# Performance work log

Hardware: AMD Instinct MI355X
Metric: run time of the kernel (lower is better)

## Reference

```python
import jax, jax.numpy as jnp
import numpy as np

NU, NI, NB, D = 100000, 50000, 20000, 64
E_UI, E_UB, E_BI = 1_000_000, 600_000, 400_000
BATCH = 2048
NUM_LAYERS = 2
C_TEMP = 0.25


def _sym_laplacian(src, dst, n_src_offset, n_total):
    # bipartite graph made symmetric: edges (u, off+v) and (off+v, u), val 1.0
    row = np.concatenate([src, n_src_offset + dst])
    col = np.concatenate([n_src_offset + dst, src])
    deg = np.bincount(row, minlength=n_total).astype(np.float64)
    val = 1.0 / ((np.sqrt(deg[row]) + 1e-8) * (np.sqrt(deg[col]) + 1e-8))
    return row.astype(np.int32), col.astype(np.int32), val.astype(np.float32)


def setup_inputs() -> dict:
    rng = np.random.default_rng(0)
    ui_u = rng.integers(0, NU, E_UI)
    ui_i = rng.integers(0, NI, E_UI)
    ub_u = rng.integers(0, NU, E_UB)
    ub_b = rng.integers(0, NB, E_UB)
    bi_b = rng.integers(0, NB, E_BI)
    bi_i = rng.integers(0, NI, E_BI)

    il_row, il_col, il_val = _sym_laplacian(ui_u, ui_i, NU, NU + NI)
    bl_row, bl_col, bl_val = _sym_laplacian(ub_u, ub_b, NU, NU + NB)
    deg_b = np.bincount(bi_b, minlength=NB).astype(np.float64)
    agg_val = (1.0 / (deg_b + 1e-8))[bi_b].astype(np.float32)

    key = jax.random.key(0)
    k1, k2, k3 = jax.random.split(key, 3)
    std = 0.05  # xavier-ish init scale
    return {
        "users_feature": jax.random.normal(k1, (NU, D), jnp.float32) * std,
        "items_feature": jax.random.normal(k2, (NI, D), jnp.float32) * std,
        "bundles_feature": jax.random.normal(k3, (NB, D), jnp.float32) * std,
        "il_row": jnp.asarray(il_row), "il_col": jnp.asarray(il_col), "il_val": jnp.asarray(il_val),
        "bl_row": jnp.asarray(bl_row), "bl_col": jnp.asarray(bl_col), "bl_val": jnp.asarray(bl_val),
        "agg_row": jnp.asarray(bi_b.astype(np.int32)), "agg_col": jnp.asarray(bi_i.astype(np.int32)),
        "agg_val": jnp.asarray(agg_val),
        "users": jnp.asarray(rng.integers(0, NU, BATCH).astype(np.int32)),
        "bundles": jnp.asarray(rng.integers(0, NB, (BATCH, 2)).astype(np.int32)),
    }


def _spmm(row, col, val, feat, n):
    # COO SpMM: out[r] += val * feat[c]   (gather + segment-sum, memory bound)
    return jax.ops.segment_sum(val[:, None] * feat[col], row, num_segments=n)


def _one_propagate(row, col, val, A, B):
    f = jnp.concatenate([A, B], axis=0)
    n = f.shape[0]
    acc = f
    for i in range(NUM_LAYERS):
        f = _spmm(row, col, val, f, n) / (i + 2)
        nrm = jnp.maximum(jnp.linalg.norm(f, axis=1, keepdims=True), 1e-12)
        acc = acc + f / nrm
    return acc[: A.shape[0]], acc[A.shape[0]:]


def _c_loss(pos, aug):
    pos = pos / jnp.maximum(jnp.linalg.norm(pos, axis=1, keepdims=True), 1e-12)
    aug = aug / jnp.maximum(jnp.linalg.norm(aug, axis=1, keepdims=True), 1e-12)
    pos_score = jnp.sum(pos * aug, axis=1) / C_TEMP
    ttl = (pos @ aug.T) / C_TEMP
    return -jnp.mean(pos_score - jax.scipy.special.logsumexp(ttl, axis=1))


def reference(users_feature, items_feature, bundles_feature,
              il_row, il_col, il_val, bl_row, bl_col, bl_val,
              agg_row, agg_col, agg_val, users, bundles):
    # item-level propagation over symmetric (U+I) graph
    IL_u, IL_i = _one_propagate(il_row, il_col, il_val, users_feature, items_feature)
    # bundle rep from item-level: row-normalized [B,I] spmm
    IL_b = _spmm(agg_row, agg_col, agg_val, IL_i, bundles_feature.shape[0])
    # bundle-level propagation over symmetric (U+B) graph
    BL_u, BL_b = _one_propagate(bl_row, bl_col, bl_val, users_feature, bundles_feature)

    # BPR on (pos, neg) bundle pairs, summing both views
    pred = (jnp.sum(IL_u[users][:, None, :] * IL_b[bundles], axis=-1)
            + jnp.sum(BL_u[users][:, None, :] * BL_b[bundles], axis=-1))  # [BATCH, 2]
    bpr_loss = jnp.mean(jax.nn.softplus(pred[:, 1] - pred[:, 0]))  # -log sigmoid(pos-neg)

    c_loss = 0.5 * (_c_loss(IL_u[users], BL_u[users]) + _c_loss(IL_b[bundles[:, 0]], BL_b[bundles[:, 0]]))
    return jnp.stack([bpr_loss, c_loss])
```

## Files before the change

### kernel.cpp

```cpp
#include <hip/hip_runtime.h>
#include <hip/hip_fp16.h>
#include <math.h>

#define DD 64
#define INV_TEMP 4.0f
#define MAXBINS 1280
#define BINSHIFT 8
#define CAP 10240
#define ECAP2 (CAP / 512)
#define ECAP_A 16
#define COLBITS 18
#define COLMASK ((1u << COLBITS) - 1)
#define CBSHIFT 14
#define K1 32.0f
#define K2_OVER_K1 4.0f

typedef float v2f __attribute__((ext_vector_type(2)));

__device__ __forceinline__ float waveSum(float x) {
#pragma unroll
    for (int off = 32; off > 0; off >>= 1) x += __shfl_xor(x, off, 64);
    return x;
}

__device__ __forceinline__ unsigned packH2(float a, float b) {
    __half2 h = __halves2half2(__float2half_rn(a), __float2half_rn(b));
    return *(unsigned*)&h;
}
__device__ __forceinline__ float2 unpackH2(unsigned u) {
    __half2 h = *(__half2*)&u;
    return __half22float2(h);
}
__device__ __forceinline__ unsigned packFp8x4(float a, float b, float c, float d) {
    int v = __builtin_amdgcn_cvt_pk_fp8_f32(a, b, 0, false);
    v = __builtin_amdgcn_cvt_pk_fp8_f32(c, d, v, true);
    return (unsigned)v;
}

__device__ __forceinline__ void accFp8(uint4 d,
    v2f& a0, v2f& a1, v2f& a2, v2f& a3,
    v2f& a4, v2f& a5, v2f& a6, v2f& a7)
{
    a0 += __builtin_amdgcn_cvt_pk_f32_fp8((int)d.x, false);
    a1 += __builtin_amdgcn_cvt_pk_f32_fp8((int)d.x, true);
    a2 += __builtin_amdgcn_cvt_pk_f32_fp8((int)d.y, false);
    a3 += __builtin_amdgcn_cvt_pk_f32_fp8((int)d.y, true);
    a4 += __builtin_amdgcn_cvt_pk_f32_fp8((int)d.z, false);
    a5 += __builtin_amdgcn_cvt_pk_f32_fp8((int)d.z, true);
    a6 += __builtin_amdgcn_cvt_pk_f32_fp8((int)d.w, false);
    a7 += __builtin_amdgcn_cvt_pk_f32_fp8((int)d.w, true);
}

__device__ __forceinline__ void accH16(uint4 d,
    v2f& a0, v2f& a1, v2f& a2, v2f& a3)
{
    float2 h0 = unpackH2(d.x), h1 = unpackH2(d.y);
    float2 h2 = unpackH2(d.z), h3 = unpackH2(d.w);
    a0[0] += h0.x; a0[1] += h0.y; a1[0] += h1.x; a1[1] += h1.y;
    a2[0] += h2.x; a2[1] += h2.y; a3[0] += h3.x; a3[1] += h3.y;
}

__device__ __forceinline__ void zero4(uint4& d) { d.x = 0; d.y = 0; d.z = 0; d.w = 0; }

__device__ __forceinline__ void gatherFp8(
    const int* __restrict__ csp, int deg,
    const unsigned* __restrict__ tab, int sub,
    v2f& a0, v2f& a1, v2f& a2, v2f& a3,
    v2f& a4, v2f& a5, v2f& a6, v2f& a7)
{
    if (deg <= 0) return;
    int c0 = csp[0];
    int c1 = (1 < deg) ? csp[1] : 0;
    int c2 = (2 < deg) ? csp[2] : 0;
    int c3 = (3 < deg) ? csp[3] : 0;
    int c4 = (4 < deg) ? csp[4] : 0;
    int c5 = (5 < deg) ? csp[5] : 0;
    int c6 = (6 < deg) ? csp[6] : 0;
    int c7 = (7 < deg) ? csp[7] : 0;
    int kc = 0, k = 8;
    while (true) {
        uint4 d0 = *((const uint4*)(tab + (size_t)c0 * 16) + sub);
        uint4 d1 = *((const uint4*)(tab + (size_t)c1 * 16) + sub);
        uint4 d2 = *((const uint4*)(tab + (size_t)c2 * 16) + sub);
        uint4 d3 = *((const uint4*)(tab + (size_t)c3 * 16) + sub);
        uint4 d4 = *((const uint4*)(tab + (size_t)c4 * 16) + sub);
        uint4 d5 = *((const uint4*)(tab + (size_t)c5 * 16) + sub);
        uint4 d6 = *((const uint4*)(tab + (size_t)c6 * 16) + sub);
        uint4 d7 = *((const uint4*)(tab + (size_t)c7 * 16) + sub);
        bool more = k < deg;
        int n0 = 0, n1 = 0, n2 = 0, n3 = 0, n4 = 0, n5 = 0, n6 = 0, n7 = 0;
        if (more) {
            n0 = csp[k];
            n1 = (k + 1 < deg) ? csp[k + 1] : 0;
            n2 = (k + 2 < deg) ? csp[k + 2] : 0;
            n3 = (k + 3 < deg) ? csp[k + 3] : 0;
            n4 = (k + 4 < deg) ? csp[k + 4] : 0;
            n5 = (k + 5 < deg) ? csp[k + 5] : 0;
            n6 = (k + 6 < deg) ? csp[k + 6] : 0;
            n7 = (k + 7 < deg) ? csp[k + 7] : 0;
        }
        if (kc + 1 >= deg) zero4(d1);
        if (kc + 2 >= deg) zero4(d2);
        if (kc + 3 >= deg) zero4(d3);
        if (kc + 4 >= deg) zero4(d4);
        if (kc + 5 >= deg) zero4(d5);
        if (kc + 6 >= deg) zero4(d6);
        if (kc + 7 >= deg) zero4(d7);
        accFp8(d0, a0, a1, a2, a3, a4, a5, a6, a7);
        accFp8(d1, a0, a1, a2, a3, a4, a5, a6, a7);
        accFp8(d2, a0, a1, a2, a3, a4, a5, a6, a7);
        accFp8(d3, a0, a1, a2, a3, a4, a5, a6, a7);
        accFp8(d4, a0, a1, a2, a3, a4, a5, a6, a7);
        accFp8(d5, a0, a1, a2, a3, a4, a5, a6, a7);
        accFp8(d6, a0, a1, a2, a3, a4, a5, a6, a7);
        accFp8(d7, a0, a1, a2, a3, a4, a5, a6, a7);
        if (!more) break;
        c0 = n0; c1 = n1; c2 = n2; c3 = n3;
        c4 = n4; c5 = n5; c6 = n6; c7 = n7;
        kc = k; k += 8;
    }
}


__device__ __forceinline__ void fetchEdge(
    int i, const int* __restrict__ r1, const int* __restrict__ c1,
    const int* __restrict__ r2, const int* __restrict__ c2,
    const int* __restrict__ r3, const int* __restrict__ c3,
    int E1, int E12, int b2, int b3, int& row, int& col)
{
    if (i < E1)       { row = __builtin_nontemporal_load(&r1[i]);
                        col = __builtin_nontemporal_load(&c1[i]); }
    else if (i < E12) { int j = i - E1;
                        row = b2 + __builtin_nontemporal_load(&r2[j]);
                        col = __builtin_nontemporal_load(&c2[j]); }
    else              { int j = i - E12;
                        row = b3 + __builtin_nontemporal_load(&r3[j]);
                        col = __builtin_nontemporal_load(&c3[j]); }
}

__global__ void __launch_bounds__(1024)
binA_kernel(
    const int* __restrict__ r1, const int* __restrict__ c1,
    const int* __restrict__ r2, const int* __restrict__ c2,
    const int* __restrict__ r3, const int* __restrict__ c3,
    int E1, int E2, int E3, int b2, int b3, int nbins,
    int* __restrict__ binCursor, unsigned* __restrict__ binned,
    int chunk, int Etot)
{
    __shared__ int hist[MAXBINS];
    __shared__ int resv[MAXBINS];
    int t = threadIdx.x;
    for (int b = t; b < nbins; b += 1024) hist[b] = 0;
    __syncthreads();
    int lo = blockIdx.x * chunk;
    int hi = min(lo + chunk, Etot);
    int E12 = E1 + E2;
    int rowR[ECAP_A], colR[ECAP_A];
#pragma unroll
    for (int j = 0; j < ECAP_A; j++) {
        int i = lo + t + (j << 10);
        if (i < hi) {
            int row, col;
            fetchEdge(i, r1, c1, r2, c2, r3, c3, E1, E12, b2, b3, row, col);
            rowR[j] = row; colR[j] = col;
            atomicAdd(&hist[row >> BINSHIFT], 1);
        }
    }
    __syncthreads();
    for (int b = t; b < nbins; b += 1024) {
        int h = hist[b];
        resv[b] = h ? atomicAdd(&binCursor[b], h) : 0;
    }
    __syncthreads();
    for (int b = t; b < nbins; b += 1024) hist[b] = 0;
    __syncthreads();
#pragma unroll
    for (int j = 0; j < ECAP_A; j++) {
        int i = lo + t + (j << 10);
        if (i < hi) {
            int row = rowR[j], col = colR[j];
            int b = row >> BINSHIFT;
            int off = atomicAdd(&hist[b], 1);
            unsigned v = ((unsigned)(row & 255) << COLBITS) | (unsigned)col;
            binned[(size_t)b * CAP + resv[b] + off] = v;
        }
    }
}

__global__ void __launch_bounds__(512) binB_kernel(
    unsigned* __restrict__ binned, const int* __restrict__ binCursor,
    int ntot,
    int* __restrict__ cnt, int* __restrict__ rowStart)
{
    __shared__ int hist[4096];
    __shared__ int tsum[512];
    __shared__ int wtot[8];
    int b = blockIdx.x;
    size_t base = (size_t)b * CAP;
    int len = min(binCursor[b], CAP);
    int rowLo = b << BINSHIFT;
    int t = threadIdx.x;
#pragma unroll
    for (int i = 0; i < 8; i++) hist[t * 8 + i] = 0;
    __syncthreads();

    unsigned ent[ECAP2];
#pragma unroll
    for (int k = 0; k < ECAP2; k++) {
        int i = t + (k << 9);
        if (i < len) {
            unsigned u = __builtin_nontemporal_load(&binned[base + i]);
            ent[k] = u;
            int key = (int)((u >> COLBITS) << 4) | (int)((u & COLMASK) >> CBSHIFT);
            atomicAdd(&hist[key], 1);
        }
    }
    __syncthreads();

    int s0, s1, s2, s3, s4, s5, s6, s7;
    int b8 = t * 8;
    s0 = hist[b8];     s1 = hist[b8 + 1]; s2 = hist[b8 + 2]; s3 = hist[b8 + 3];
    s4 = hist[b8 + 4]; s5 = hist[b8 + 5]; s6 = hist[b8 + 6]; s7 = hist[b8 + 7];
    int tot = s0 + s1 + s2 + s3 + s4 + s5 + s6 + s7;
    int lane = t & 63, w = t >> 6;
    int sc = tot;
    for (int off = 1; off < 64; off <<= 1) {
        int u = __shfl_up(sc, off, 64);
        if (lane >= off) sc += u;
    }
    if (lane == 63) wtot[w] = sc;
    __syncthreads();
    int woff = 0;
    for (int i = 0; i < w; i++) woff += wtot[i];
    int run = woff + sc - tot;
    hist[b8] = run;     run += s0;
    hist[b8 + 1] = run; run += s1;
    hist[b8 + 2] = run; run += s2;
    hist[b8 + 3] = run; run += s3;
    hist[b8 + 4] = run; run += s4;
    hist[b8 + 5] = run; run += s5;
    hist[b8 + 6] = run; run += s6;
    hist[b8 + 7] = run;
    __syncthreads();

    int grow = rowLo + t;
    if (t < 256 && grow < ntot) {
        int rs = hist[t << 4];
        int nx = (t == 255) ? len : hist[(t + 1) << 4];
        cnt[grow] = nx - rs;
        rowStart[grow] = (int)base + rs;
    }
    __syncthreads();

#pragma unroll
    for (int k = 0; k < ECAP2; k++) {
        int i = t + (k << 9);
        if (i < len) {
            unsigned u = ent[k];
            int key = (int)((u >> COLBITS) << 4) | (int)((u & COLMASK) >> CBSHIFT);
            int p = atomicAdd(&hist[key], 1);
            binned[base + p] = u & COLMASK;
        }
    }
}

__global__ void __launch_bounds__(256) prep_kernel(
    const float* __restrict__ usersF, const float* __restrict__ itemsF,
    const float* __restrict__ bundF, const int* __restrict__ cnt,
    int NUv, int NIv, int NBv, int n1,
    unsigned* __restrict__ g01, unsigned* __restrict__ g02,
    unsigned* __restrict__ hfeat)
{
    int total = (NUv + NIv + NBv) * 16;
    int stride = gridDim.x * blockDim.x;
    for (int idx = blockIdx.x * blockDim.x + threadIdx.x; idx < total; idx += stride) {
        int rl = idx >> 4, pr = idx & 15;
        float4 f;
        if (rl < NUv) {
            f = *((const float4*)(usersF + (size_t)rl * DD) + pr);
            float s1 = K1 / (sqrtf((float)cnt[rl]) + 1e-8f);
            float s2 = K1 / (sqrtf((float)cnt[n1 + rl]) + 1e-8f);
            g01[(size_t)rl * 16 + pr] = packFp8x4(f.x*s1, f.y*s1, f.z*s1, f.w*s1);
            g02[(size_t)rl * 16 + pr] = packFp8x4(f.x*s2, f.y*s2, f.z*s2, f.w*s2);
        } else if (rl < NUv + NIv) {
            int r = rl - NUv;
            f = *((const float4*)(itemsF + (size_t)r * DD) + pr);
            float s = K1 / (sqrtf((float)cnt[NUv + r]) + 1e-8f);
            g01[(size_t)(NUv + r) * 16 + pr] = packFp8x4(f.x*s, f.y*s, f.z*s, f.w*s);
        } else {
            int r = rl - NUv - NIv;
            f = *((const float4*)(bundF + (size_t)r * DD) + pr);
            float s = K1 / (sqrtf((float)cnt[n1 + NUv + r]) + 1e-8f);
            g02[(size_t)(NUv + r) * 16 + pr] = packFp8x4(f.x*s, f.y*s, f.z*s, f.w*s);
        }
        uint2 h;
        h.x = packH2(f.x, f.y);
        h.y = packH2(f.z, f.w);
        *(uint2*)(hfeat + (size_t)rl * 32 + pr * 2) = h;
    }
}

__global__ void __launch_bounds__(256) spmm_l1(
    const int* __restrict__ rowStart, const int* __restrict__ cnt,
    const int* __restrict__ cs, int n1, int nAll,
    const unsigned* __restrict__ g01, const unsigned* __restrict__ g02,
    unsigned* __restrict__ g11, unsigned* __restrict__ g12,
    __half* __restrict__ nrm11, __half* __restrict__ nrm12)
{
    int lane = threadIdx.x & 63;
    int grp  = lane >> 2;
    int sub  = lane & 3;
    int wave = (blockIdx.x * blockDim.x + threadIdx.x) >> 6;
    int nW   = (gridDim.x * blockDim.x) >> 6;
    for (int g0 = wave * 16; g0 < nAll; g0 += nW * 16) {
        int g = g0 + grp;
        bool valid = g < nAll;
        int gi = valid ? g : nAll - 1;
        int start = rowStart[gi];
        int deg   = valid ? cnt[gi] : 0;
        bool first = gi < n1;
        const unsigned* tab = first ? g01 : g02;
        v2f a0 = {0.f,0.f}, a1 = {0.f,0.f}, a2 = {0.f,0.f}, a3 = {0.f,0.f};
        v2f a4 = {0.f,0.f}, a5 = {0.f,0.f}, a6 = {0.f,0.f}, a7 = {0.f,0.f};
        gatherFp8(cs + start, deg, tab, sub, a0, a1, a2, a3, a4, a5, a6, a7);
        float ns = a0[0]*a0[0] + a0[1]*a0[1] + a1[0]*a1[0] + a1[1]*a1[1]
                 + a2[0]*a2[0] + a2[1]*a2[1] + a3[0]*a3[0] + a3[1]*a3[1]
                 + a4[0]*a4[0] + a4[1]*a4[1] + a5[0]*a5[0] + a5[1]*a5[1]
                 + a6[0]*a6[0] + a6[1]*a6[1] + a7[0]*a7[0] + a7[1]*a7[1];
        ns += __shfl_xor(ns, 1, 64);
        ns += __shfl_xor(ns, 2, 64);
        float inv = 1.0f / fmaxf(sqrtf(ns), 1e-12f);
        float s = 1.0f / (sqrtf((float)deg) + 1e-8f);
        float m = K2_OVER_K1 * s * s;
        if (valid) {
            int r = first ? g : g - n1;
            unsigned* o8p = first ? g11 + (size_t)r * 16
                                  : g12 + (size_t)r * 16;
            __half* o16p = first ? nrm11 + (size_t)r * DD
                                 : nrm12 + (size_t)r * DD;
            uint4 o8;
            o8.x = packFp8x4(a0[0]*m, a0[1]*m, a1[0]*m, a1[1]*m);
            o8.y = packFp8x4(a2[0]*m, a2[1]*m, a3[0]*m, a3[1]*m);
            o8.z = packFp8x4(a4[0]*m, a4[1]*m, a5[0]*m, a5[1]*m);
            o8.w = packFp8x4(a6[0]*m, a6[1]*m, a7[0]*m, a7[1]*m);
            *((uint4*)o8p + sub) = o8;
            uint4 oA, oB;
            oA.x = packH2(a0[0]*inv, a0[1]*inv);
            oA.y = packH2(a1[0]*inv, a1[1]*inv);
            oA.z = packH2(a2[0]*inv, a2[1]*inv);
            oA.w = packH2(a3[0]*inv, a3[1]*inv);
            oB.x = packH2(a4[0]*inv, a4[1]*inv);
            oB.y = packH2(a5[0]*inv, a5[1]*inv);
            oB.z = packH2(a6[0]*inv, a6[1]*inv);
            oB.w = packH2(a7[0]*inv, a7[1]*inv);
            *((uint4*)o16p + sub * 2)     = oA;
            *((uint4*)o16p + sub * 2 + 1) = oB;
        }
    }
}

__global__ void __launch_bounds__(256) spmm_l2(
    const int* __restrict__ rowStart, const int* __restrict__ cnt,
    const int* __restrict__ cs, int n1, int nAll, int NUv,
    const unsigned* __restrict__ g11, const unsigned* __restrict__ g12,
    const unsigned* __restrict__ hfeat,
    const __half* __restrict__ nrm11, const __half* __restrict__ nrm12,
    __half* __restrict__ accIL, __half* __restrict__ accBL)
{
    int lane = threadIdx.x & 63;
    int grp  = lane >> 2;
    int sub  = lane & 3;
    int wave = (blockIdx.x * blockDim.x + threadIdx.x) >> 6;
    int nW   = (gridDim.x * blockDim.x) >> 6;
    for (int g0 = wave * 16; g0 < nAll; g0 += nW * 16) {
        int g = g0 + grp;
        bool valid = g < nAll;
        int gi = valid ? g : nAll - 1;
        int start = rowStart[gi];
        int deg   = valid ? cnt[gi] : 0;
        bool first = gi < n1;
        const unsigned* tab = first ? g11 : g12;
        v2f a0 = {0.f,0.f}, a1 = {0.f,0.f}, a2 = {0.f,0.f}, a3 = {0.f,0.f};
        v2f a4 = {0.f,0.f}, a5 = {0.f,0.f}, a6 = {0.f,0.f}, a7 = {0.f,0.f};
        gatherFp8(cs + start, deg, tab, sub, a0, a1, a2, a3, a4, a5, a6, a7);
        float ns = a0[0]*a0[0] + a0[1]*a0[1] + a1[0]*a1[0] + a1[1]*a1[1]
                 + a2[0]*a2[0] + a2[1]*a2[1] + a3[0]*a3[0] + a3[1]*a3[1]
                 + a4[0]*a4[0] + a4[1]*a4[1] + a5[0]*a5[0] + a5[1]*a5[1]
                 + a6[0]*a6[0] + a6[1]*a6[1] + a7[0]*a7[0] + a7[1]*a7[1];
        ns += __shfl_xor(ns, 1, 64);
        ns += __shfl_xor(ns, 2, 64);
        float inv = 1.0f / fmaxf(sqrtf(ns), 1e-12f);
        if (valid) {
            int r = first ? g : g - n1;
            const unsigned* hf =
                first ? hfeat + (size_t)g * 32
                      : ((r < NUv) ? hfeat + (size_t)r * 32
                                   : hfeat + (size_t)(n1 + (r - NUv)) * 32);
            const __half* nrmIn = first ? nrm11 + (size_t)r * DD
                                        : nrm12 + (size_t)r * DD;
            __half* outp = first ? accIL + (size_t)r * DD
                                 : accBL + (size_t)r * DD;
            uint4 fA = *((const uint4*)hf + sub * 2);
            uint4 fB = *((const uint4*)hf + sub * 2 + 1);
            float2 f0 = unpackH2(fA.x), f1 = unpackH2(fA.y);
            float2 f2 = unpackH2(fA.z), f3 = unpackH2(fA.w);
            float2 f4 = unpackH2(fB.x), f5 = unpackH2(fB.y);
            float2 f6 = unpackH2(fB.z), f7 = unpackH2(fB.w);
            uint4 nvA = *((const uint4*)nrmIn + sub * 2);
            uint4 nvB = *((const uint4*)nrmIn + sub * 2 + 1);
            float2 m0 = unpackH2(nvA.x), m1 = unpackH2(nvA.y);
            float2 m2 = unpackH2(nvA.z), m3 = unpackH2(nvA.w);
            float2 m4 = unpackH2(nvB.x), m5 = unpackH2(nvB.y);
            float2 m6 = unpackH2(nvB.z), m7 = unpackH2(nvB.w);
            uint4 oA, oB;
            oA.x = packH2(f0.x + m0.x + a0[0]*inv, f0.y + m0.y + a0[1]*inv);
            oA.y = packH2(f1.x + m1.x + a1[0]*inv, f1.y + m1.y + a1[1]*inv);
            oA.z = packH2(f2.x + m2.x + a2[0]*inv, f2.y + m2.y + a2[1]*inv);
            oA.w = packH2(f3.x + m3.x + a3[0]*inv, f3.y + m3.y + a3[1]*inv);
            oB.x = packH2(f4.x + m4.x + a4[0]*inv, f4.y + m4.y + a4[1]*inv);
            oB.y = packH2(f5.x + m5.x + a5[0]*inv, f5.y + m5.y + a5[1]*inv);
            oB.z = packH2(f6.x + m6.x + a6[0]*inv, f6.y + m6.y + a6[1]*inv);
            oB.w = packH2(f7.x + m7.x + a7[0]*inv, f7.y + m7.y + a7[1]*inv);
            *((uint4*)outp + sub * 2)     = oA;
            *((uint4*)outp + sub * 2 + 1) = oB;
        }
    }
}

__global__ void __launch_bounds__(256) spmm_agg(
    const int* __restrict__ rowStart, const int* __restrict__ cnt,
    const int* __restrict__ cs, int rbase,
    const __half* __restrict__ table16, __half* __restrict__ out16, int n)
{
    int lane = threadIdx.x & 63;
    int grp  = lane >> 3;
    int sub  = lane & 7;
    int wave = (blockIdx.x * blockDim.x + threadIdx.x) >> 6;
    int nW   = (gridDim.x * blockDim.x) >> 6;
    for (int r0 = wave * 8; r0 < n; r0 += nW * 8) {
        int r = r0 + grp;
        bool valid = r < n;
        int idx = rbase + (valid ? r : n - 1);
        int start = rowStart[idx];
        int deg   = valid ? cnt[idx] : 0;
        const int* csp = cs + start;
        v2f a0 = {0.f, 0.f}, a1 = {0.f, 0.f}, a2 = {0.f, 0.f}, a3 = {0.f, 0.f};
        if (deg > 0) {
            int c0 = csp[0];
            int c1i = (1 < deg) ? csp[1] : 0;
            int c2i = (2 < deg) ? csp[2] : 0;
            int c3i = (3 < deg) ? csp[3] : 0;
            int kc = 0, k = 4;
            while (true) {
                uint4 d0 = *((const uint4*)(table16 + (size_t)c0 * DD) + sub);
                uint4 d1 = *((const uint4*)(table16 + (size_t)c1i * DD) + sub);
                uint4 d2 = *((const uint4*)(table16 + (size_t)c2i * DD) + sub);
                uint4 d3 = *((const uint4*)(table16 + (size_t)c3i * DD) + sub);
                bool more = k < deg;
                int n0 = 0, n1v = 0, n2v = 0, n3v = 0;
                if (more) {
                    n0  = csp[k];
                    n1v = (k + 1 < deg) ? csp[k + 1] : 0;
                    n2v = (k + 2 < deg) ? csp[k + 2] : 0;
                    n3v = (k + 3 < deg) ? csp[k + 3] : 0;
                }
                if (kc + 1 >= deg) zero4(d1);
                if (kc + 2 >= deg) zero4(d2);
                if (kc + 3 >= deg) zero4(d3);
                accH16(d0, a0, a1, a2, a3);
                accH16(d1, a0, a1, a2, a3);
                accH16(d2, a0, a1, a2, a3);
                accH16(d3, a0, a1, a2, a3);
                if (!more) break;
                c0 = n0; c1i = n1v; c2i = n2v; c3i = n3v;
                kc = k; k += 4;
            }
        }
        float sc2 = 1.0f / ((float)deg + 1e-8f);
        if (valid) {
            uint4 o;
            o.x = packH2(a0[0]*sc2, a0[1]*sc2);
            o.y = packH2(a1[0]*sc2, a1[1]*sc2);
            o.z = packH2(a2[0]*sc2, a2[1]*sc2);
            o.w = packH2(a3[0]*sc2, a3[1]*sc2);
            *((uint4*)(out16 + (size_t)r * DD) + sub) = o;
        }
    }
}


__global__ void batch_kernel(
    const int* __restrict__ users, const int* __restrict__ bundles,
    const __half* __restrict__ IL, const __half* __restrict__ ILb,
    const __half* __restrict__ BL, int NUv,
    float* __restrict__ pos1, float* __restrict__ aug1,
    float* __restrict__ pos2, float* __restrict__ aug2,
    float* __restrict__ sums, int batch)
{
    int lane = threadIdx.x & 63;
    int wave = (blockIdx.x * blockDim.x + threadIdx.x) >> 6;
    int nW   = (gridDim.x * blockDim.x) >> 6;
    for (int b = wave; b < batch; b += nW) {
        int u   = users[b];
        int bp  = bundles[2 * b];
        int bn  = bundles[2 * b + 1];
        float ilu  = __half2float(IL [(size_t)u * DD + lane]);
        float blu  = __half2float(BL [(size_t)u * DD + lane]);
        float ilb0 = __half2float(ILb[(size_t)bp * DD + lane]);
        float ilb1 = __half2float(ILb[(size_t)bn * DD + lane]);
        float blb0 = __half2float(BL [(size_t)(NUv + bp) * DD + lane]);
        float blb1 = __half2float(BL [(size_t)(NUv + bn) * DD + lane]);
        float d0 = waveSum(ilu * ilb0 + blu * blb0);
        float d1 = waveSum(ilu * ilb1 + blu * blb1);
        float x  = d1 - d0;
        float sp = fmaxf(x, 0.f) + log1pf(expf(-fabsf(x)));
        if (lane == 0) atomicAdd(&sums[0], sp);
        float nilu = sqrtf(waveSum(ilu * ilu));
        float nblu = sqrtf(waveSum(blu * blu));
        float nilb = sqrtf(waveSum(ilb0 * ilb0));
        float nblb = sqrtf(waveSum(blb0 * blb0));
        pos1[(size_t)b * DD + lane] = ilu  / fmaxf(nilu, 1e-12f);
        aug1[(size_t)b * DD + lane] = blu  / fmaxf(nblu, 1e-12f);
        pos2[(size_t)b * DD + lane] = ilb0 / fmaxf(nilb, 1e-12f);
        aug2[(size_t)b * DD + lane] = blb0 / fmaxf(nblb, 1e-12f);
    }
}

__device__ __forceinline__ void load_tile_T(const float* __restrict__ src, int rowBase,
                                            int batch, float* __restrict__ dst, int tx) {
    int i = tx >> 2, c = tx & 3;
#pragma unroll
    for (int t = 0; t < 4; t++) {
        int k0 = c * 4 + t * 16;
        float4 v = make_float4(0.f, 0.f, 0.f, 0.f);
        int gi = rowBase + i;
        if (gi < batch) v = *(const float4*)&src[(size_t)gi * DD + k0];
        dst[(k0 + 0) * 68 + i] = v.x;
        dst[(k0 + 1) * 68 + i] = v.y;
        dst[(k0 + 2) * 68 + i] = v.z;
        dst[(k0 + 3) * 68 + i] = v.w;
    }
}

__global__ void closs_kernel(
    const float* __restrict__ pos1, const float* __restrict__ aug1,
    const float* __restrict__ pos2, const float* __restrict__ aug2,
    float* __restrict__ S, float* __restrict__ Dg, int batch, int jChunk)
{
    const float* pos = blockIdx.z ? pos2 : pos1;
    const float* aug = blockIdx.z ? aug2 : aug1;
    __shared__ float Pt[64 * 68];
    __shared__ float At[64 * 68];
    __shared__ float red[64 * 17];
    int tx = threadIdx.x;
    int iBase = blockIdx.x * 64;
    int jBeg = blockIdx.y * jChunk;
    int jEnd = min(jBeg + jChunk, batch);
    load_tile_T(pos, iBase, batch, Pt, tx);
    int tr = tx >> 4, tc = tx & 15;
    float rs[4] = {0.f, 0.f, 0.f, 0.f};
    for (int j0 = jBeg; j0 < jEnd; j0 += 64) {
        __syncthreads();
        load_tile_T(aug, j0, batch, At, tx);
        __syncthreads();
        float acc[16];
#pragma unroll
        for (int q = 0; q < 16; q++) acc[q] = 0.f;
#pragma unroll 8
        for (int k = 0; k < 64; k++) {
            float4 pv = *(const float4*)&Pt[k * 68 + 4 * tr];
            float4 av = *(const float4*)&At[k * 68 + 4 * tc];
            acc[0]  += pv.x * av.x;  acc[1]  += pv.x * av.y;
            acc[2]  += pv.x * av.z;  acc[3]  += pv.x * av.w;
            acc[4]  += pv.y * av.x;  acc[5]  += pv.y * av.y;
            acc[6]  += pv.y * av.z;  acc[7]  += pv.y * av.w;
            acc[8]  += pv.z * av.x;  acc[9]  += pv.z * av.y;
            acc[10] += pv.z * av.z;  acc[11] += pv.z * av.w;
            acc[12] += pv.w * av.x;  acc[13] += pv.w * av.y;
            acc[14] += pv.w * av.z;  acc[15] += pv.w * av.w;
        }
#pragma unroll
        for (int qi = 0; qi < 4; qi++) {
            int gi = iBase + 4 * tr + qi;
#pragma unroll
            for (int qj = 0; qj < 4; qj++) {
                int gj = j0 + 4 * tc + qj;
                float t = acc[qi * 4 + qj] * INV_TEMP;
                if (gi < batch && gj < batch) {
                    rs[qi] += __expf(t);
                    if (gi == gj) Dg[blockIdx.z * batch + gi] = t;
                }
            }
        }
    }
    __syncthreads();
#pragma unroll
    for (int qi = 0; qi < 4; qi++) red[(4 * tr + qi) * 17 + tc] = rs[qi];
    __syncthreads();
    if (tx < 64) {
        float s = 0.f;
#pragma unroll
        for (int c = 0; c < 16; c++) s += red[tx * 17 + c];
        int gi = iBase + tx;
        if (gi < batch) atomicAdd(&S[blockIdx.z * batch + gi], s);
    }
}

__global__ void closs_finish(const float* __restrict__ S, const float* __restrict__ Dg,
                             const float* __restrict__ sums,
                             float* __restrict__ out, int batch, float invB)
{
    int tid = threadIdx.x;
    __shared__ float wsm[2][4];
    float tot[2];
#pragma unroll
    for (int m = 0; m < 2; m++) {
        float local = 0.f;
        for (int i = tid; i < batch; i += blockDim.x)
            local += logf(S[m * batch + i]) - Dg[m * batch + i];
        local = waveSum(local);
        if ((tid & 63) == 0) wsm[m][tid >> 6] = local;
    }
    __syncthreads();
    if (tid == 0) {
#pragma unroll
        for (int m = 0; m < 2; m++)
            tot[m] = wsm[m][0] + wsm[m][1] + wsm[m][2] + wsm[m][3];
        out[0] = sums[0] * invB;
        out[1] = 0.5f * (tot[0] + tot[1]) * invB;
    }
}


extern "C" void kernel_launch(void* const* d_in, const int* in_sizes, int n_in,
                              void* d_out, int out_size, void* d_ws, size_t ws_size,
                              hipStream_t stream)
{
    const float* usersF = (const float*)d_in[0];
    const float* itemsF = (const float*)d_in[1];
    const float* bundF  = (const float*)d_in[2];
    const int*   il_row = (const int*)d_in[3];
    const int*   il_col = (const int*)d_in[4];
    const int*   bl_row = (const int*)d_in[6];
    const int*   bl_col = (const int*)d_in[7];
    const int*   agg_row = (const int*)d_in[9];
    const int*   agg_col = (const int*)d_in[10];
    const int*   users   = (const int*)d_in[12];
    const int*   bundles = (const int*)d_in[13];

    const int NUv = in_sizes[0] / DD;
    const int NIv = in_sizes[1] / DD;
    const int NBv = in_sizes[2] / DD;
    const int E1 = in_sizes[3], E2 = in_sizes[6], E3 = in_sizes[9];
    const int batch = in_sizes[12];
    const int n1 = NUv + NIv;
    const int n2 = NUv + NBv;
    const int ntot = n1 + n2 + NBv;
    const int Etot = E1 + E2 + E3;
    const int nbins = (ntot + 255) >> BINSHIFT;

    float* ws = (float*)d_ws;
    size_t off = 0;
    float* sums = ws + off;      off += 16;
    float* S    = ws + off;      off += (size_t)2 * batch;
    float* Dg   = ws + off;      off += (size_t)2 * batch;
    float* pos1 = ws + off;      off += (size_t)batch * DD;
    float* aug1 = ws + off;      off += (size_t)batch * DD;
    float* pos2 = ws + off;      off += (size_t)batch * DD;
    float* aug2 = ws + off;      off += (size_t)batch * DD;
    int*   cnt  = (int*)(ws + off);      off += (size_t)ntot;
    int*   rowStart = (int*)(ws + off);  off += (size_t)ntot;
    int*   binCursor = (int*)(ws + off); off += MAXBINS;
    off = (off + 3) & ~(size_t)3;
    unsigned* binned = (unsigned*)(ws + off); off += (size_t)nbins * CAP;
    unsigned* g01 = (unsigned*)(ws + off); off += (size_t)n1 * 16;
    unsigned* g11 = (unsigned*)(ws + off); off += (size_t)n1 * 16;
    unsigned* g02 = (unsigned*)(ws + off); off += (size_t)n2 * 16;
    unsigned* g12 = (unsigned*)(ws + off); off += (size_t)n2 * 16;
    unsigned* hfeat = (unsigned*)(ws + off); off += (size_t)(n1 + NBv) * 32;
    off = (off + 3) & ~(size_t)3;
    __half* hbase = (__half*)(ws + off);
    size_t hoff = 0;
    __half* nrm11 = hbase + hoff;  hoff += (size_t)n1 * DD;
    __half* accIL = hbase + hoff;  hoff += (size_t)n1 * DD;
    __half* nrm12 = hbase + hoff;  hoff += (size_t)n2 * DD;
    __half* accBL = hbase + hoff;  hoff += (size_t)n2 * DD;
    __half* ILb   = hbase + hoff;  hoff += (size_t)NBv * DD;
    (void)ws_size;

    hipMemsetAsync(sums, 0, 16 * sizeof(float), stream);
    hipMemsetAsync(S, 0, (size_t)2 * batch * sizeof(float), stream);
    hipMemsetAsync(binCursor, 0, MAXBINS * sizeof(int), stream);

    int nA = (Etot + ECAP_A * 1024 - 1) / (ECAP_A * 1024);
    if (nA < 256) nA = 256;
    int chunk = (Etot + nA - 1) / nA;
    binA_kernel<<<nA, 1024, 0, stream>>>(
        il_row, il_col, bl_row, bl_col, agg_row, agg_col,
        E1, E2, E3, n1, n1 + n2, nbins, binCursor, binned, chunk, Etot);
    binB_kernel<<<nbins, 512, 0, stream>>>(
        binned, binCursor, ntot, cnt, rowStart);

    prep_kernel<<<2048, 256, 0, stream>>>(
        usersF, itemsF, bundF, cnt, NUv, NIv, NBv, n1, g01, g02, hfeat);

    const int* cs = (const int*)binned;
    const int nAll = n1 + n2;

    auto grid16 = [](int n) { return (n + 63) / 64; };
    auto grid8  = [](int n) { return (n + 31) / 32; };

    spmm_l1<<<grid16(nAll), 256, 0, stream>>>(
        rowStart, cnt, cs, n1, nAll, g01, g02, g11, g12, nrm11, nrm12);

    spmm_l2<<<grid16(nAll), 256, 0, stream>>>(
        rowStart, cnt, cs, n1, nAll, NUv, g11, g12,
        hfeat, nrm11, nrm12, accIL, accBL);

    spmm_agg<<<grid8(NBv), 256, 0, stream>>>(
        rowStart, cnt, cs, n1 + n2, accIL + (size_t)NUv * DD, ILb, NBv);

    batch_kernel<<<(batch + 3) / 4, 256, 0, stream>>>(
        users, bundles, accIL, ILb, accBL, NUv,
        pos1, aug1, pos2, aug2, sums, batch);

    const int yChunks = 8;
    int jChunk = ((batch + yChunks * 64 - 1) / (yChunks * 64)) * 64;
    dim3 cg2((batch + 63) / 64, yChunks, 2);
    closs_kernel<<<cg2, 256, 0, stream>>>(pos1, aug1, pos2, aug2, S, Dg, batch, jChunk);
    closs_finish<<<1, 256, 0, stream>>>(S, Dg, sums, (float*)d_out, batch,
                                        1.0f / (float)batch);
}
```

Before: 359.7 us.

## Compute contrastive-loss similarity matrix with fp16 MFMA instead of scalar FMA

The normalized batch embeddings are now stored in fp16, and the 2048x2048 similarity products in the contrastive loss are computed with 16x16x32 f16 MFMA instructions. Fragments are loaded directly from global memory, so the LDS tiling and block syncs are gone. Row sums of exp are reduced across lanes with shuffles and added with atomics, and the j-split drops from 8 chunks to 4. This cuts the FMA work of a compute-bound stage and halves its memory traffic, at the cost of fp16 precision in the logits.

```diff
diff --git a/kernel.cpp b/kernel.cpp
--- a/kernel.cpp
+++ b/kernel.cpp
@@ -16,6 +16,9 @@
 #define K2_OVER_K1 4.0f
 
 typedef float v2f __attribute__((ext_vector_type(2)));
+typedef _Float16 f16x4v __attribute__((ext_vector_type(4)));
+typedef _Float16 f16x8v __attribute__((ext_vector_type(8)));
+typedef float f32x4v __attribute__((ext_vector_type(4)));
 
 __device__ __forceinline__ float waveSum(float x) {
 #pragma unroll
@@ -193,7 +196,6 @@
     int* __restrict__ cnt, int* __restrict__ rowStart)
 {
     __shared__ int hist[4096];
-    __shared__ int tsum[512];
     __shared__ int wtot[8];
     int b = blockIdx.x;
     size_t base = (size_t)b * CAP;
@@ -493,8 +495,8 @@
     const int* __restrict__ users, const int* __restrict__ bundles,
     const __half* __restrict__ IL, const __half* __restrict__ ILb,
     const __half* __restrict__ BL, int NUv,
-    float* __restrict__ pos1, float* __restrict__ aug1,
-    float* __restrict__ pos2, float* __restrict__ aug2,
+    __half* __restrict__ pos1, __half* __restrict__ aug1,
+    __half* __restrict__ pos2, __half* __restrict__ aug2,
     float* __restrict__ sums, int batch)
 {
     int lane = threadIdx.x & 63;
@@ -519,90 +521,72 @@
         float nblu = sqrtf(waveSum(blu * blu));
         float nilb = sqrtf(waveSum(ilb0 * ilb0));
         float nblb = sqrtf(waveSum(blb0 * blb0));
-        pos1[(size_t)b * DD + lane] = ilu  / fmaxf(nilu, 1e-12f);
-        aug1[(size_t)b * DD + lane] = blu  / fmaxf(nblu, 1e-12f);
-        pos2[(size_t)b * DD + lane] = ilb0 / fmaxf(nilb, 1e-12f);
-        aug2[(size_t)b * DD + lane] = blb0 / fmaxf(nblb, 1e-12f);
-    }
-}
-
-__device__ __forceinline__ void load_tile_T(const float* __restrict__ src, int rowBase,
-                                            int batch, float* __restrict__ dst, int tx) {
-    int i = tx >> 2, c = tx & 3;
-#pragma unroll
-    for (int t = 0; t < 4; t++) {
-        int k0 = c * 4 + t * 16;
-        float4 v = make_float4(0.f, 0.f, 0.f, 0.f);
-        int gi = rowBase + i;
-        if (gi < batch) v = *(const float4*)&src[(size_t)gi * DD + k0];
-        dst[(k0 + 0) * 68 + i] = v.x;
-        dst[(k0 + 1) * 68 + i] = v.y;
-        dst[(k0 + 2) * 68 + i] = v.z;
-        dst[(k0 + 3) * 68 + i] = v.w;
-    }
-}
-
-__global__ void closs_kernel(
-    const float* __restrict__ pos1, const float* __restrict__ aug1,
-    const float* __restrict__ pos2, const float* __restrict__ aug2,
+        pos1[(size_t)b * DD + lane] = __float2half(ilu  / fmaxf(nilu, 1e-12f));
+        aug1[(size_t)b * DD + lane] = __float2half(blu  / fmaxf(nblu, 1e-12f));
+        pos2[(size_t)b * DD + lane] = __float2half(ilb0 / fmaxf(nilb, 1e-12f));
+        aug2[(size_t)b * DD + lane] = __float2half(blb0 / fmaxf(nblb, 1e-12f));
+    }
+}
+
+__device__ __forceinline__ f16x8v loadFrag(const __half* rowp, int g, int k0) {
+    const _Float16* p = (const _Float16*)rowp;
+    f16x4v lo = *(const f16x4v*)(p + k0 + 4 * g);
+    f16x4v hi = *(const f16x4v*)(p + k0 + 16 + 4 * g);
+    f16x8v r;
+    r[0] = lo[0]; r[1] = lo[1]; r[2] = lo[2]; r[3] = lo[3];
+    r[4] = hi[0]; r[5] = hi[1]; r[6] = hi[2]; r[7] = hi[3];
+    return r;
+}
+
+__global__ void __launch_bounds__(256) closs_kernel(
+    const __half* __restrict__ pos1, const __half* __restrict__ aug1,
+    const __half* __restrict__ pos2, const __half* __restrict__ aug2,
     float* __restrict__ S, float* __restrict__ Dg, int batch, int jChunk)
 {
-    const float* pos = blockIdx.z ? pos2 : pos1;
-    const float* aug = blockIdx.z ? aug2 : aug1;
-    __shared__ float Pt[64 * 68];
-    __shared__ float At[64 * 68];
-    __shared__ float red[64 * 17];
-    int tx = threadIdx.x;
-    int iBase = blockIdx.x * 64;
+    int view = blockIdx.z;
+    const __half* pos = view ? pos2 : pos1;
+    const __half* aug = view ? aug2 : aug1;
+    int w = threadIdx.x >> 6, lane = threadIdx.x & 63;
+    int g = lane >> 4, c = lane & 15;
+    int i0 = blockIdx.x * 64 + w * 16;
     int jBeg = blockIdx.y * jChunk;
     int jEnd = min(jBeg + jChunk, batch);
-    load_tile_T(pos, iBase, batch, Pt, tx);
-    int tr = tx >> 4, tc = tx & 15;
-    float rs[4] = {0.f, 0.f, 0.f, 0.f};
-    for (int j0 = jBeg; j0 < jEnd; j0 += 64) {
-        __syncthreads();
-        load_tile_T(aug, j0, batch, At, tx);
-        __syncthreads();
-        float acc[16];
-#pragma unroll
-        for (int q = 0; q < 16; q++) acc[q] = 0.f;
-#pragma unroll 8
-        for (int k = 0; k < 64; k++) {
-            float4 pv = *(const float4*)&Pt[k * 68 + 4 * tr];
-            float4 av = *(const float4*)&At[k * 68 + 4 * tc];
-            acc[0]  += pv.x * av.x;  acc[1]  += pv.x * av.y;
-            acc[2]  += pv.x * av.z;  acc[3]  += pv.x * av.w;
-            acc[4]  += pv.y * av.x;  acc[5]  += pv.y * av.y;
-            acc[6]  += pv.y * av.z;  acc[7]  += pv.y * av.w;
-            acc[8]  += pv.z * av.x;  acc[9]  += pv.z * av.y;
-            acc[10] += pv.z * av.z;  acc[11] += pv.z * av.w;
-            acc[12] += pv.w * av.x;  acc[13] += pv.w * av.y;
-            acc[14] += pv.w * av.z;  acc[15] += pv.w * av.w;
-        }
-#pragma unroll
-        for (int qi = 0; qi < 4; qi++) {
-            int gi = iBase + 4 * tr + qi;
-#pragma unroll
-            for (int qj = 0; qj < 4; qj++) {
-                int gj = j0 + 4 * tc + qj;
-                float t = acc[qi * 4 + qj] * INV_TEMP;
-                if (gi < batch && gj < batch) {
-                    rs[qi] += __expf(t);
-                    if (gi == gj) Dg[blockIdx.z * batch + gi] = t;
-                }
-            }
-        }
-    }
-    __syncthreads();
-#pragma unroll
-    for (int qi = 0; qi < 4; qi++) red[(4 * tr + qi) * 17 + tc] = rs[qi];
-    __syncthreads();
-    if (tx < 64) {
-        float s = 0.f;
-#pragma unroll
-        for (int c = 0; c < 16; c++) s += red[tx * 17 + c];
-        int gi = iBase + tx;
-        if (gi < batch) atomicAdd(&S[blockIdx.z * batch + gi], s);
+    int ra = min(i0 + c, batch - 1);
+    const __half* prow = pos + (size_t)ra * DD;
+    f16x8v aF0 = loadFrag(prow, g, 0);
+    f16x8v aF1 = loadFrag(prow, g, 32);
+    float rs0 = 0.f, rs1 = 0.f, rs2 = 0.f, rs3 = 0.f;
+    for (int j0 = jBeg; j0 < jEnd; j0 += 16) {
+        int rb = min(j0 + c, batch - 1);
+        const __half* arow = aug + (size_t)rb * DD;
+        f16x8v bF0 = loadFrag(arow, g, 0);
+        f16x8v bF1 = loadFrag(arow, g, 32);
+        f32x4v acc = {0.f, 0.f, 0.f, 0.f};
+        acc = __builtin_amdgcn_mfma_f32_16x16x32_f16(aF0, bF0, acc, 0, 0, 0);
+        acc = __builtin_amdgcn_mfma_f32_16x16x32_f16(aF1, bF1, acc, 0, 0, 0);
+        int gj = j0 + c;
+#pragma unroll
+        for (int e = 0; e < 4; e++) {
+            int gi = i0 + g * 4 + e;
+            float t = acc[e] * INV_TEMP;
+            float ex = (gi < batch && gj < batch) ? __expf(t) : 0.f;
+            if (gi == gj && gi < batch) Dg[view * batch + gi] = t;
+            ex += __shfl_xor(ex, 1, 64);
+            ex += __shfl_xor(ex, 2, 64);
+            ex += __shfl_xor(ex, 4, 64);
+            ex += __shfl_xor(ex, 8, 64);
+            if (e == 0) rs0 += ex;
+            else if (e == 1) rs1 += ex;
+            else if (e == 2) rs2 += ex;
+            else rs3 += ex;
+        }
+    }
+    if (c == 0) {
+        int base = view * batch + i0 + g * 4;
+        if (base - view * batch + 0 < batch) atomicAdd(&S[base + 0], rs0);
+        if (base - view * batch + 1 < batch) atomicAdd(&S[base + 1], rs1);
+        if (base - view * batch + 2 < batch) atomicAdd(&S[base + 2], rs2);
+        if (base - view * batch + 3 < batch) atomicAdd(&S[base + 3], rs3);
     }
 }
 
@@ -664,10 +648,6 @@
     float* sums = ws + off;      off += 16;
     float* S    = ws + off;      off += (size_t)2 * batch;
     float* Dg   = ws + off;      off += (size_t)2 * batch;
-    float* pos1 = ws + off;      off += (size_t)batch * DD;
-    float* aug1 = ws + off;      off += (size_t)batch * DD;
-    float* pos2 = ws + off;      off += (size_t)batch * DD;
-    float* aug2 = ws + off;      off += (size_t)batch * DD;
     int*   cnt  = (int*)(ws + off);      off += (size_t)ntot;
     int*   rowStart = (int*)(ws + off);  off += (size_t)ntot;
     int*   binCursor = (int*)(ws + off); off += MAXBINS;
@@ -686,6 +666,10 @@
     __half* nrm12 = hbase + hoff;  hoff += (size_t)n2 * DD;
     __half* accBL = hbase + hoff;  hoff += (size_t)n2 * DD;
     __half* ILb   = hbase + hoff;  hoff += (size_t)NBv * DD;
+    __half* pos1  = hbase + hoff;  hoff += (size_t)batch * DD;
+    __half* aug1  = hbase + hoff;  hoff += (size_t)batch * DD;
+    __half* pos2  = hbase + hoff;  hoff += (size_t)batch * DD;
+    __half* aug2  = hbase + hoff;  hoff += (size_t)batch * DD;
     (void)ws_size;
 
     hipMemsetAsync(sums, 0, 16 * sizeof(float), stream);
@@ -724,8 +708,8 @@
         users, bundles, accIL, ILb, accBL, NUv,
         pos1, aug1, pos2, aug2, sums, batch);
 
-    const int yChunks = 8;
-    int jChunk = ((batch + yChunks * 64 - 1) / (yChunks * 64)) * 64;
+    const int yChunks = 4;
+    int jChunk = ((batch + yChunks * 16 - 1) / (yChunks * 16)) * 16;
     dim3 cg2((batch + 63) / 64, yChunks, 2);
     closs_kernel<<<cg2, 256, 0, stream>>>(pos1, aug1, pos2, aug2, S, Dg, batch, jChunk);
     closs_finish<<<1, 256, 0, stream>>>(S, Dg, sums, (float*)d_out, batch,
```

Result: no change. 365.8 us (+1.7%).
